# Performance work log

Measured on AMD Instinct MI355X. Metric: run time of the kernel, lower is better.

Reference implementation:

```python
import jax, jax.numpy as jnp
import numpy as np

B, S, D, H, K = 16, 4096, 256, 512, 3
EPS = 1e-5


def setup_inputs() -> dict:
    key = jax.random.key(0)
    ks = jax.random.split(key, 16)
    glorot = lambda k, shape: jax.random.uniform(
        k, shape, jnp.float32, -1.0, 1.0) * np.sqrt(6.0 / (shape[0] + shape[-1]))
    return {
        "inputs": jax.random.normal(ks[0], (B, S, D), jnp.float32),
        "mask": jax.random.randint(ks[1], (B, S), 0, 2, jnp.int32),
        "in_w": glorot(ks[2], (H, D)),
        "in_b": jnp.zeros((H,), jnp.float32),
        "gate_w": glorot(ks[3], (H, D)),
        "gate_b": jnp.zeros((H,), jnp.float32),
        "dw_w": glorot(ks[4], (H, 1, K)),
        "dw_b": jnp.zeros((H,), jnp.float32),
        "pw_w": glorot(ks[5], (H, H, 1)),
        "pw_b": jnp.zeros((H,), jnp.float32),
        "ln_g": jnp.ones((H,), jnp.float32),
        "ln_b": jnp.zeros((H,), jnp.float32),
        "A_log": jax.random.normal(ks[6], (H,), jnp.float32) * -0.1,
        "Bp": jax.random.normal(ks[7], (H,), jnp.float32) * 0.1,
        "Cp": jax.random.normal(ks[8], (H,), jnp.float32) * 0.1,
    }


def _forward(inputs, mask, in_w, in_b, gate_w, gate_b, dw_w, dw_b,
             pw_w, pw_b, ln_g, ln_b, A_log, Bp, Cp):
    # projections: torch Linear is x @ W.T + b
    x_lin = jnp.einsum('bsd,hd->bsh', inputs, in_w) + in_b
    g_lin = jnp.einsum('bsd,hd->bsh', inputs, gate_w) + gate_b
    h = jnp.tanh(x_lin)
    m_f = mask.astype(h.dtype)                      # [B,S]
    h = h * m_f[:, :, None]
    # depthwise conv over time: [B,H,S] with groups=H, 'same' padding
    pad = (K - 1) // 2
    h_t = jnp.transpose(h, (0, 2, 1))               # [B,H,S]
    h_conv = jax.lax.conv_general_dilated(
        h_t, dw_w, window_strides=(1,), padding=[(pad, pad)],
        dimension_numbers=('NCH', 'OIH', 'NCH'), feature_group_count=H)
    h_conv = h_conv + dw_b[None, :, None]
    h_conv = jnp.transpose(h_conv, (0, 2, 1))       # [B,S,H]
    # pointwise 1x1 conv
    h_conv = jnp.einsum('bsh,oh->bso', h_conv, pw_w[:, :, 0]) + pw_b
    u = jax.nn.silu(h_conv + h)
    g = jax.nn.sigmoid(g_lin)
    a_exp = jnp.exp(-jax.nn.softplus(A_log))        # [H]

    def step(carry, xs):
        state, last = carry
        ut, gt, mt = xs                             # [B,H],[B,H],[B]
        new_state = gt * (a_exp * state) + (1.0 - gt) * (Bp * ut)
        keep = (mt > 0.5)[:, None]
        state = jnp.where(keep, new_state, state)
        y = state * Cp
        last = jnp.where(keep, y, last)
        return (state, last), last

    init = (jnp.zeros((B, H), u.dtype), jnp.zeros((B, H), u.dtype))
    xs = (jnp.transpose(u, (1, 0, 2)), jnp.transpose(g, (1, 0, 2)),
          jnp.transpose(m_f, (1, 0)))
    _, y_seq = jax.lax.scan(step, init, xs)         # [S,B,H]
    y_seq = jnp.transpose(y_seq, (1, 0, 2))         # [B,S,H]
    # LayerNorm over last dim
    mu = jnp.mean(y_seq, axis=-1, keepdims=True)
    var = jnp.var(y_seq, axis=-1, keepdims=True)
    return (y_seq - mu) * jax.lax.rsqrt(var + EPS) * ln_g + ln_b


def reference(inputs, mask, in_w, in_b, gate_w, gate_b, dw_w, dw_b,
              pw_w, pw_b, ln_g, ln_b, A_log, Bp, Cp):
    return _forward(inputs, mask, in_w, in_b, gate_w, gate_b, dw_w, dw_b,
                    pw_w, pw_b, ln_g, ln_b, A_log, Bp, Cp)
```

## Files before the change

### kernel.cpp

```cpp
#include <hip/hip_runtime.h>
#include <hip/hip_bf16.h>
#include <math.h>

#define B_  16
#define S_  4096
#define D_  256
#define H_  512
#define BS_ 65536
#define BSH_ 33554432L
#define BSD_ 16777216L
#define CCH 128
#define LCH 32
#define TPAD 136

typedef __bf16 bf16;
typedef __bf16 bf16x8 __attribute__((ext_vector_type(8)));
typedef float  f32x4  __attribute__((ext_vector_type(4)));

#define AS1 __attribute__((address_space(1)))
#define AS3 __attribute__((address_space(3)))

__device__ __forceinline__ void gload_lds16(const void* g, void* l) {
  __builtin_amdgcn_global_load_lds((const AS1 void*)g, (AS3 void*)l, 16, 0, 0);
}

#if __has_builtin(__builtin_amdgcn_exp2f)
#define EXP2F __builtin_amdgcn_exp2f
#else
#define EXP2F exp2f
#endif
#if __has_builtin(__builtin_amdgcn_rcpf)
#define RCPF __builtin_amdgcn_rcpf
#else
#define RCPF(x) (1.f/(x))
#endif
#define L2E 1.4426950408889634f

__device__ __forceinline__ float fsigmoid(float x) {
  return RCPF(1.f + EXP2F(-L2E * x));
}
__device__ __forceinline__ float ftanh(float x) {
  return 2.f * RCPF(1.f + EXP2F(-2.f * L2E * x)) - 1.f;
}
__device__ __forceinline__ float fsilu(float x) {
  return x * RCPF(1.f + EXP2F(-L2E * x));
}

__global__ void k_cast_x(const float* __restrict__ x, bf16* __restrict__ xb, int n8) {
  int i = blockIdx.x * blockDim.x + threadIdx.x;
  if (i >= n8) return;
  const float4* p = (const float4*)x + (long)i * 2;
  float4 a = p[0], b = p[1];
  bf16x8 o;
  o[0]=(bf16)a.x; o[1]=(bf16)a.y; o[2]=(bf16)a.z; o[3]=(bf16)a.w;
  o[4]=(bf16)b.x; o[5]=(bf16)b.y; o[6]=(bf16)b.z; o[7]=(bf16)b.w;
  ((bf16x8*)xb)[i] = o;
}

__global__ void k_cast_w(const float* __restrict__ in_w, const float* __restrict__ gate_w,
                         const float* __restrict__ pw_w,
                         bf16* __restrict__ w1, bf16* __restrict__ pw) {
  int i = blockIdx.x * blockDim.x + threadIdx.x;
  const int HD = H_ * D_;
  if (i < HD)            w1[i] = (bf16)in_w[i];
  else if (i < 2 * HD)   w1[i] = (bf16)gate_w[i - HD];
  else {
    int j = i - 2 * HD;
    if (j < H_ * H_)     pw[j] = (bf16)pw_w[j];
  }
}

template<int KDIM, int EPI>
__global__ __launch_bounds__(512, 5)
void k_gemm(const bf16* __restrict__ A, const bf16* __restrict__ Bw,
            const int* __restrict__ mask,
            const float* __restrict__ bias0, const float* __restrict__ bias1,
            const bf16* __restrict__ hbuf, const bf16* __restrict__ gbuf,
            const float* __restrict__ A_log, const float* __restrict__ Bp,
            float* __restrict__ Ac, float* __restrict__ Bc,
            bf16* __restrict__ out0, bf16* __restrict__ out1, int Ntiles)
{
  extern __shared__ char smem_raw[];
  bf16* tile = (bf16*)smem_raw;

  const int t = threadIdx.x;
  const int w = t >> 6, lane = t & 63;
  const int nwg = gridDim.x;
  const int wg = (blockIdx.x & 7) * (nwg >> 3) + (blockIdx.x >> 3);
  const int bn0 = (wg % Ntiles) * 128;
  const int bm0 = (wg / Ntiles) * 128;
  const int wm = w >> 2, wn = w & 3;
  const int fr = lane & 15, kq = lane >> 4;
  constexpr int NT = KDIM / 32;

  const bf16* Ag = A  + (long)(bm0 + (t >> 2)) * KDIM + (t & 3) * 8;
  const bf16* Bg = Bw + (long)(bn0 + (t >> 2)) * KDIM + (t & 3) * 8;

  f32x4 acc[4][2];
#pragma unroll
  for (int i = 0; i < 4; ++i)
#pragma unroll
    for (int j = 0; j < 2; ++j) acc[i][j] = (f32x4){0.f, 0.f, 0.f, 0.f};

#define STAGE(tt)                                                           \
  { char* _b = smem_raw + ((tt) & 1) * 16384;                               \
    gload_lds16(Ag + (tt) * 32, (bf16*)_b + t * 8);                         \
    gload_lds16(Bg + (tt) * 32, (bf16*)(_b + 8192) + t * 8); }

  STAGE(0); STAGE(1);

#pragma unroll
  for (int kt = 0; kt < NT; ++kt) {
    if (kt + 1 < NT) asm volatile("s_waitcnt vmcnt(2)" ::: "memory");
    else             asm volatile("s_waitcnt vmcnt(0)" ::: "memory");
    __builtin_amdgcn_s_barrier();

    const bf16* As = (const bf16*)(smem_raw + (kt & 1) * 16384);
    const bf16* Bs = As + 4096;
    bf16x8 af[4], bfr[2];
#pragma unroll
    for (int mi = 0; mi < 4; ++mi)
      af[mi] = *(const bf16x8*)&As[(wm * 64 + mi * 16 + fr) * 32 + kq * 8];
#pragma unroll
    for (int ni = 0; ni < 2; ++ni)
      bfr[ni] = *(const bf16x8*)&Bs[(wn * 32 + ni * 16 + fr) * 32 + kq * 8];

    asm volatile("s_waitcnt lgkmcnt(0)" ::: "memory");
    __builtin_amdgcn_s_barrier();

    if (kt + 2 < NT) STAGE(kt + 2);

#pragma unroll
    for (int mi = 0; mi < 4; ++mi)
#pragma unroll
      for (int ni = 0; ni < 2; ++ni)
        acc[mi][ni] = __builtin_amdgcn_mfma_f32_16x16x32_bf16(af[mi], bfr[ni], acc[mi][ni], 0, 0, 0);
  }
#undef STAGE

  __syncthreads();

  const bool hside = (EPI != 1) || (bn0 < H_);
#pragma unroll
  for (int mi = 0; mi < 4; ++mi) {
#pragma unroll
    for (int rr = 0; rr < 4; ++rr) {
      const int row = wm * 64 + mi * 16 + kq * 4 + rr;
      const int gm = bm0 + row;
      float mf = 1.f;
      if (EPI == 1) mf = (mask[gm] != 0) ? 1.f : 0.f;
#pragma unroll
      for (int ni = 0; ni < 2; ++ni) {
        const int col = wn * 32 + ni * 16 + fr;
        float c = acc[mi][ni][rr];
        float val;
        if (EPI == 1) {
          const int gn = bn0 + col;
          val = hside ? ftanh(c + bias0[gn]) * mf
                      : fsigmoid(c + bias1[gn - H_]);
        } else {
          val = c + bias0[bn0 + col];
        }
        tile[row * TPAD + col] = (bf16)val;
      }
    }
  }
  __syncthreads();

  const int pr = t >> 4;
  const int pc = (t & 15) * 8;
#pragma unroll
  for (int rr = 0; rr < 4; ++rr) {
    const int row = pr + rr * 32;
    const long gm = bm0 + row;
    bf16x8 v = *(const bf16x8*)&tile[row * TPAD + pc];
    if (EPI == 1) {
      if (hside) *(bf16x8*)&out0[gm * H_ + bn0 + pc] = v;
      else       *(bf16x8*)&out1[gm * H_ + (bn0 - H_) + pc] = v;
    } else {
      bf16x8 hb = *(const bf16x8*)&hbuf[gm * H_ + bn0 + pc];
      bf16x8 o;
#pragma unroll
      for (int k = 0; k < 8; ++k) {
        float s = (float)v[k] + (float)hb[k];
        o[k] = (bf16)fsilu(s);
      }
      *(bf16x8*)&out0[gm * H_ + bn0 + pc] = o;
      *(bf16x8*)&tile[row * TPAD + pc] = o;
    }
  }

  if constexpr (EPI == 2) {
    __syncthreads();
    const int c_idx = t >> 7;
    const int col   = t & 127;
    const int gcol  = bn0 + col;
    const int bIdx  = bm0 >> 12;
    const int s0    = bm0 & (S_ - 1);
    const int chunk = (s0 >> 5) + c_idx;
    const int* mrow = mask + bIdx * S_ + s0 + c_idx * 32;
    const float aexp = RCPF(1.f + EXP2F(L2E * A_log[gcol]));
    const float bp = Bp[gcol];
    const bf16* grow = gbuf + (long)(bm0 + c_idx * 32) * H_ + gcol;
    float At = 1.f, Bt = 0.f;
#pragma unroll 4
    for (int sl = 0; sl < LCH; ++sl) {
      float uv = (float)tile[(c_idx * 32 + sl) * TPAD + col];
      float gv = (float)grow[(long)sl * H_];
      bool mm = mrow[sl] != 0;
      float a_s = mm ? gv * aexp : 1.f;
      float b_s = mm ? (1.f - gv) * (bp * uv) : 0.f;
      At = a_s * At;
      Bt = fmaf(a_s, Bt, b_s);
    }
    long o = ((long)chunk * B_ + bIdx) * H_ + gcol;
    Ac[o] = At; Bc[o] = Bt;
  }
}

__global__ void k_dwconv(const bf16* __restrict__ h, const float* __restrict__ dww,
                         const float* __restrict__ dwb, bf16* __restrict__ hc)
{
  long idx = (long)blockIdx.x * blockDim.x + threadIdx.x;
  long m = idx >> 6;
  int h8 = ((int)idx & 63) << 3;
  int s = (int)(m & (S_ - 1));
  bf16x8 c0, c1, c2;
#pragma unroll
  for (int j = 0; j < 8; ++j) { c0[j] = (bf16)0.f; c2[j] = (bf16)0.f; }
  if (s > 0)        c0 = *(const bf16x8*)(h + (m - 1) * H_ + h8);
  c1 = *(const bf16x8*)(h + m * H_ + h8);
  if (s < S_ - 1)   c2 = *(const bf16x8*)(h + (m + 1) * H_ + h8);
  bf16x8 o;
#pragma unroll
  for (int j = 0; j < 8; ++j) {
    int hh = h8 + j;
    float v = (float)c0[j] * dww[hh * 3 + 0] + (float)c1[j] * dww[hh * 3 + 1]
            + (float)c2[j] * dww[hh * 3 + 2] + dwb[hh];
    o[j] = (bf16)v;
  }
  *(bf16x8*)(hc + m * H_ + h8) = o;
}


__global__ __launch_bounds__(256)
void k_scan2(const float* __restrict__ Ac, const float* __restrict__ Bc,
             float* __restrict__ Sin)
{
  int tid = blockIdx.x * 256 + threadIdx.x;
  int b = tid >> 9, h = tid & (H_ - 1);
  const long stride = (long)B_ * H_;
  long o = (long)b * H_ + h;
  float st = 0.f;
  float a = Ac[o], bb = Bc[o];
  for (int c = 0; c < CCH; ++c) {
    float an = 0.f, bn = 0.f;
    if (c + 1 < CCH) { an = Ac[o + stride]; bn = Bc[o + stride]; }
    Sin[o] = st;
    st = fmaf(a, st, bb);
    a = an; bb = bn; o += stride;
  }
}

__global__ __launch_bounds__(256)
void k_scan3(const bf16* __restrict__ u, const bf16* __restrict__ g,
             const int* __restrict__ mask, const float* __restrict__ A_log,
             const float* __restrict__ Bp, const float* __restrict__ Cp,
             const float* __restrict__ Sin,
             const float* __restrict__ ln_g, const float* __restrict__ ln_b,
             float* __restrict__ out)
{
  const int wv = threadIdx.x >> 6, lane = threadIdx.x & 63;
  const int c = blockIdx.x * 4 + wv;
  const int b = blockIdx.y;
  const int h0 = lane * 8;

  float aexp[8], bp[8], cp[8], lg[8], lb[8], st[8];
#pragma unroll
  for (int j = 0; j < 8; ++j) {
    aexp[j] = RCPF(1.f + EXP2F(L2E * A_log[h0 + j]));
    bp[j] = Bp[h0 + j]; cp[j] = Cp[h0 + j];
    lg[j] = ln_g[h0 + j]; lb[j] = ln_b[h0 + j];
    st[j] = Sin[((long)c * B_ + b) * H_ + h0 + j];
  }

  const long base = ((long)b * S_ + (long)c * LCH) * H_ + h0;
  const int* mrow = mask + b * S_ + c * LCH;

  bf16x8 uv = *(const bf16x8*)(u + base);
  bf16x8 gv = *(const bf16x8*)(g + base);
  int mm = mrow[0];

  for (int sl = 0; sl < LCH; ++sl) {
    bf16x8 un, gn; int mn = 0;
    if (sl + 1 < LCH) {
      un = *(const bf16x8*)(u + base + (long)(sl + 1) * H_);
      gn = *(const bf16x8*)(g + base + (long)(sl + 1) * H_);
      mn = mrow[sl + 1];
    }
    const bool m = mm != 0;
    float y[8], sum = 0.f, sq = 0.f;
#pragma unroll
    for (int j = 0; j < 8; ++j) {
      float uu = (float)uv[j], gg = (float)gv[j];
      float a_s = m ? gg * aexp[j] : 1.f;
      float b_s = m ? (1.f - gg) * (bp[j] * uu) : 0.f;
      st[j] = fmaf(a_s, st[j], b_s);
      y[j] = st[j] * cp[j];
      sum += y[j];
      sq = fmaf(y[j], y[j], sq);
    }
#pragma unroll
    for (int off = 32; off; off >>= 1) {
      sum += __shfl_xor(sum, off);
      sq  += __shfl_xor(sq, off);
    }
    const float mu = sum * (1.f / H_);
    const float var = sq * (1.f / H_) - mu * mu;
    const float rs = rsqrtf(var + 1e-5f);
    const long ob = base + (long)sl * H_;
    f32x4 o0, o1;
#pragma unroll
    for (int j = 0; j < 4; ++j) o0[j] = (y[j] - mu) * rs * lg[j] + lb[j];
#pragma unroll
    for (int j = 0; j < 4; ++j) o1[j] = (y[4 + j] - mu) * rs * lg[4 + j] + lb[4 + j];
    *(f32x4*)(out + ob) = o0;
    *(f32x4*)(out + ob + 4) = o1;
    uv = un; gv = gn; mm = mn;
  }
}

extern "C" void kernel_launch(void* const* d_in, const int* in_sizes, int n_in,
                              void* d_out, int out_size, void* d_ws, size_t ws_size,
                              hipStream_t stream)
{
  const float* x      = (const float*)d_in[0];
  const int*   mask   = (const int*)d_in[1];
  const float* in_w   = (const float*)d_in[2];
  const float* in_b   = (const float*)d_in[3];
  const float* gate_w = (const float*)d_in[4];
  const float* gate_b = (const float*)d_in[5];
  const float* dw_w   = (const float*)d_in[6];
  const float* dw_b   = (const float*)d_in[7];
  const float* pw_w   = (const float*)d_in[8];
  const float* pw_b   = (const float*)d_in[9];
  const float* ln_g   = (const float*)d_in[10];
  const float* ln_b   = (const float*)d_in[11];
  const float* A_log  = (const float*)d_in[12];
  const float* Bp     = (const float*)d_in[13];
  const float* Cp     = (const float*)d_in[14];

  char* ws = (char*)d_ws;
  bf16*  xb  = (bf16*)(ws + 0L);
  bf16*  h   = (bf16*)(ws + 33554432L);
  bf16*  hc  = (bf16*)(ws + 100663296L);
  bf16*  u   = (bf16*)(ws + 167772160L);
  bf16*  g   = (bf16*)(ws + 234881024L);
  bf16*  w1  = (bf16*)(ws + 301989888L);
  bf16*  pw  = (bf16*)(ws + 302514176L);
  float* Ac  = (float*)(ws + 303038464L);
  float* Bc  = (float*)(ws + 307232768L);
  float* Sin = (float*)(ws + 311427072L);
  float* out = (float*)d_out;

  const int gemm_lds = 128 * TPAD * 2;

  k_cast_x<<<8192, 256, 0, stream>>>(x, xb, (int)(BSD_ / 8));
  k_cast_w<<<2048, 256, 0, stream>>>(in_w, gate_w, pw_w, w1, pw);
  k_gemm<256, 1><<<512 * 8, 512, gemm_lds, stream>>>(
      xb, w1, mask, in_b, gate_b, nullptr, nullptr, nullptr, nullptr,
      nullptr, nullptr, h, g, 8);
  k_dwconv<<<16384, 256, 0, stream>>>(h, dw_w, dw_b, hc);
  k_gemm<512, 2><<<512 * 4, 512, gemm_lds, stream>>>(
      hc, pw, mask, pw_b, nullptr, h, g, A_log, Bp,
      Ac, Bc, u, nullptr, 4);
  k_scan2<<<32, 256, 0, stream>>>(Ac, Bc, Sin);
  k_scan3<<<dim3(CCH / 4, B_), 256, 0, stream>>>(
      u, g, mask, A_log, Bp, Cp, Sin, ln_g, ln_b, out);
}
```

Before: 326.4 us.

## Double GEMM K-step to 64 with k-sliced LDS layout

The GEMM main loop now processes 64 K elements per stage instead of 32, halving the number of barrier/wait iterations. The LDS tile layout becomes k-slice-major (8-element columns, 128 rows contiguous) to avoid bank conflicts on fragment reads. LDS per block goes to 64KB and launch bounds drop to 4 waves per SIMD, which lowers occupancy in exchange for fewer synchronisations per FLOP.

```diff
diff --git a/kernel.cpp b/kernel.cpp
--- a/kernel.cpp
+++ b/kernel.cpp
@@ -71,7 +71,7 @@
 }
 
 template<int KDIM, int EPI>
-__global__ __launch_bounds__(512, 5)
+__global__ __launch_bounds__(512, 4)
 void k_gemm(const bf16* __restrict__ A, const bf16* __restrict__ Bw,
             const int* __restrict__ mask,
             const float* __restrict__ bias0, const float* __restrict__ bias1,
@@ -91,10 +91,13 @@
   const int bm0 = (wg / Ntiles) * 128;
   const int wm = w >> 2, wn = w & 3;
   const int fr = lane & 15, kq = lane >> 4;
-  constexpr int NT = KDIM / 32;
-
-  const bf16* Ag = A  + (long)(bm0 + (t >> 2)) * KDIM + (t & 3) * 8;
-  const bf16* Bg = Bw + (long)(bn0 + (t >> 2)) * KDIM + (t & 3) * 8;
+  constexpr int NT = KDIM / 64;
+
+  const int sr = t & 127, sk = t >> 7;
+  const bf16* Ag = A  + (long)(bm0 + sr) * KDIM + sk * 8;
+  const bf16* Bg = Bw + (long)(bn0 + sr) * KDIM + sk * 8;
+  bf16* const L0 = (bf16*)smem_raw + sk * 1024 + sr * 8;
+  bf16* const L1 = L0 + 4096;
 
   f32x4 acc[4][2];
 #pragma unroll
@@ -103,27 +106,33 @@
     for (int j = 0; j < 2; ++j) acc[i][j] = (f32x4){0.f, 0.f, 0.f, 0.f};
 
 #define STAGE(tt)                                                           \
-  { char* _b = smem_raw + ((tt) & 1) * 16384;                               \
-    gload_lds16(Ag + (tt) * 32, (bf16*)_b + t * 8);                         \
-    gload_lds16(Bg + (tt) * 32, (bf16*)(_b + 8192) + t * 8); }
+  { const int _p = ((tt) & 1) * 16384;                                      \
+    gload_lds16(Ag + (tt) * 64,      L0 + _p);                              \
+    gload_lds16(Ag + (tt) * 64 + 32, L1 + _p);                              \
+    gload_lds16(Bg + (tt) * 64,      L0 + 8192 + _p);                       \
+    gload_lds16(Bg + (tt) * 64 + 32, L1 + 8192 + _p); }
 
   STAGE(0); STAGE(1);
 
 #pragma unroll
   for (int kt = 0; kt < NT; ++kt) {
-    if (kt + 1 < NT) asm volatile("s_waitcnt vmcnt(2)" ::: "memory");
+    if (kt + 1 < NT) asm volatile("s_waitcnt vmcnt(4)" ::: "memory");
     else             asm volatile("s_waitcnt vmcnt(0)" ::: "memory");
     __builtin_amdgcn_s_barrier();
 
-    const bf16* As = (const bf16*)(smem_raw + (kt & 1) * 16384);
-    const bf16* Bs = As + 4096;
-    bf16x8 af[4], bfr[2];
-#pragma unroll
-    for (int mi = 0; mi < 4; ++mi)
-      af[mi] = *(const bf16x8*)&As[(wm * 64 + mi * 16 + fr) * 32 + kq * 8];
-#pragma unroll
-    for (int ni = 0; ni < 2; ++ni)
-      bfr[ni] = *(const bf16x8*)&Bs[(wn * 32 + ni * 16 + fr) * 32 + kq * 8];
+    const bf16* As = (const bf16*)smem_raw + (kt & 1) * 16384;
+    const bf16* Bs = As + 8192;
+    bf16x8 af[4][2], bfr[2][2];
+#pragma unroll
+    for (int kk = 0; kk < 2; ++kk) {
+      const int ks = (kk * 4 + kq) * 1024;
+#pragma unroll
+      for (int mi = 0; mi < 4; ++mi)
+        af[mi][kk] = *(const bf16x8*)&As[ks + (wm * 64 + mi * 16 + fr) * 8];
+#pragma unroll
+      for (int ni = 0; ni < 2; ++ni)
+        bfr[ni][kk] = *(const bf16x8*)&Bs[ks + (wn * 32 + ni * 16 + fr) * 8];
+    }
 
     asm volatile("s_waitcnt lgkmcnt(0)" ::: "memory");
     __builtin_amdgcn_s_barrier();
@@ -131,10 +140,12 @@
     if (kt + 2 < NT) STAGE(kt + 2);
 
 #pragma unroll
-    for (int mi = 0; mi < 4; ++mi)
-#pragma unroll
-      for (int ni = 0; ni < 2; ++ni)
-        acc[mi][ni] = __builtin_amdgcn_mfma_f32_16x16x32_bf16(af[mi], bfr[ni], acc[mi][ni], 0, 0, 0);
+    for (int kk = 0; kk < 2; ++kk)
+#pragma unroll
+      for (int mi = 0; mi < 4; ++mi)
+#pragma unroll
+        for (int ni = 0; ni < 2; ++ni)
+          acc[mi][ni] = __builtin_amdgcn_mfma_f32_16x16x32_bf16(af[mi][kk], bfr[ni][kk], acc[mi][ni], 0, 0, 0);
   }
 #undef STAGE
 
@@ -363,7 +374,7 @@
   float* Sin = (float*)(ws + 311427072L);
   float* out = (float*)d_out;
 
-  const int gemm_lds = 128 * TPAD * 2;
+  const int gemm_lds = 65536;
 
   k_cast_x<<<8192, 256, 0, stream>>>(x, xb, (int)(BSD_ / 8));
   k_cast_w<<<2048, 256, 0, stream>>>(in_w, gate_w, pw_w, w1, pw);
```

Measured after the change: 406.0 us. 1.24x slower.

## Shrink GEMM N-tile to 64 with XOR-swizzled LDS and higher occupancy

Applied to the files above, without the earlier changes.

Both GEMM kernels now use 128x64 output tiles instead of 128x128, doubling the grid and halving the per-block LDS footprint so launch bounds can request 8 blocks per CU. The LDS staging layout is XOR-swizzled on the K-quad index to reduce bank conflicts on fragment reads. The fused scan epilogue is restricted to half the threads to match the narrower tile. The smaller N tile lowers reuse of the A tile and doubles A-matrix global reads, which is traded for occupancy and load balance.

```diff
diff --git a/kernel.cpp b/kernel.cpp
--- a/kernel.cpp
+++ b/kernel.cpp
@@ -11,7 +11,7 @@
 #define BSD_ 16777216L
 #define CCH 128
 #define LCH 32
-#define TPAD 136
+#define TP  72
 
 typedef __bf16 bf16;
 typedef __bf16 bf16x8 __attribute__((ext_vector_type(8)));
@@ -71,7 +71,7 @@
 }
 
 template<int KDIM, int EPI>
-__global__ __launch_bounds__(512, 5)
+__global__ __launch_bounds__(512, 8)
 void k_gemm(const bf16* __restrict__ A, const bf16* __restrict__ Bw,
             const int* __restrict__ mask,
             const float* __restrict__ bias0, const float* __restrict__ bias1,
@@ -87,43 +87,46 @@
   const int w = t >> 6, lane = t & 63;
   const int nwg = gridDim.x;
   const int wg = (blockIdx.x & 7) * (nwg >> 3) + (blockIdx.x >> 3);
-  const int bn0 = (wg % Ntiles) * 128;
+  const int bn0 = (wg % Ntiles) * 64;
   const int bm0 = (wg / Ntiles) * 128;
   const int wm = w >> 2, wn = w & 3;
   const int fr = lane & 15, kq = lane >> 4;
+  const int kqs = (kq ^ (fr & 3)) << 3;
   constexpr int NT = KDIM / 32;
 
-  const bf16* Ag = A  + (long)(bm0 + (t >> 2)) * KDIM + (t & 3) * 8;
-  const bf16* Bg = Bw + (long)(bn0 + (t >> 2)) * KDIM + (t & 3) * 8;
-
-  f32x4 acc[4][2];
-#pragma unroll
-  for (int i = 0; i < 4; ++i)
-#pragma unroll
-    for (int j = 0; j < 2; ++j) acc[i][j] = (f32x4){0.f, 0.f, 0.f, 0.f};
-
-#define STAGE(tt)                                                           \
-  { char* _b = smem_raw + ((tt) & 1) * 16384;                               \
-    gload_lds16(Ag + (tt) * 32, (bf16*)_b + t * 8);                         \
-    gload_lds16(Bg + (tt) * 32, (bf16*)(_b + 8192) + t * 8); }
+  const int sr = t >> 2;
+  const int sq = (t & 3) ^ (sr & 3);
+  const bf16* Ag = A  + (long)(bm0 + sr) * KDIM + sq * 8;
+  const bf16* Bg = Bw + (long)(bn0 + sr) * KDIM + sq * 8;
+
+  f32x4 acc[4];
+#pragma unroll
+  for (int i = 0; i < 4; ++i) acc[i] = (f32x4){0.f, 0.f, 0.f, 0.f};
+
+#define STAGE(tt)                                                            \
+  { bf16* _b = (bf16*)smem_raw + ((tt) & 1) * 6144;                          \
+    gload_lds16(Ag + (tt) * 32, _b + t * 8);                                 \
+    if (t < 256) gload_lds16(Bg + (tt) * 32, _b + 4096 + t * 8); }
 
   STAGE(0); STAGE(1);
 
 #pragma unroll
   for (int kt = 0; kt < NT; ++kt) {
-    if (kt + 1 < NT) asm volatile("s_waitcnt vmcnt(2)" ::: "memory");
-    else             asm volatile("s_waitcnt vmcnt(0)" ::: "memory");
+    if (kt + 1 < NT) {
+      if (w < 4) asm volatile("s_waitcnt vmcnt(2)" ::: "memory");
+      else       asm volatile("s_waitcnt vmcnt(1)" ::: "memory");
+    } else {
+      asm volatile("s_waitcnt vmcnt(0)" ::: "memory");
+    }
     __builtin_amdgcn_s_barrier();
 
-    const bf16* As = (const bf16*)(smem_raw + (kt & 1) * 16384);
+    const bf16* As = (const bf16*)smem_raw + (kt & 1) * 6144;
     const bf16* Bs = As + 4096;
-    bf16x8 af[4], bfr[2];
+    bf16x8 af[4], bfr;
 #pragma unroll
     for (int mi = 0; mi < 4; ++mi)
-      af[mi] = *(const bf16x8*)&As[(wm * 64 + mi * 16 + fr) * 32 + kq * 8];
-#pragma unroll
-    for (int ni = 0; ni < 2; ++ni)
-      bfr[ni] = *(const bf16x8*)&Bs[(wn * 32 + ni * 16 + fr) * 32 + kq * 8];
+      af[mi] = *(const bf16x8*)&As[(wm * 64 + mi * 16 + fr) * 32 + kqs];
+    bfr = *(const bf16x8*)&Bs[(wn * 16 + fr) * 32 + kqs];
 
     asm volatile("s_waitcnt lgkmcnt(0)" ::: "memory");
     __builtin_amdgcn_s_barrier();
@@ -132,15 +135,14 @@
 
 #pragma unroll
     for (int mi = 0; mi < 4; ++mi)
-#pragma unroll
-      for (int ni = 0; ni < 2; ++ni)
-        acc[mi][ni] = __builtin_amdgcn_mfma_f32_16x16x32_bf16(af[mi], bfr[ni], acc[mi][ni], 0, 0, 0);
+      acc[mi] = __builtin_amdgcn_mfma_f32_16x16x32_bf16(af[mi], bfr, acc[mi], 0, 0, 0);
   }
 #undef STAGE
 
   __syncthreads();
 
   const bool hside = (EPI != 1) || (bn0 < H_);
+  const int col = wn * 16 + fr;
 #pragma unroll
   for (int mi = 0; mi < 4; ++mi) {
 #pragma unroll
@@ -149,31 +151,27 @@
       const int gm = bm0 + row;
       float mf = 1.f;
       if (EPI == 1) mf = (mask[gm] != 0) ? 1.f : 0.f;
-#pragma unroll
-      for (int ni = 0; ni < 2; ++ni) {
-        const int col = wn * 32 + ni * 16 + fr;
-        float c = acc[mi][ni][rr];
-        float val;
-        if (EPI == 1) {
-          const int gn = bn0 + col;
-          val = hside ? ftanh(c + bias0[gn]) * mf
-                      : fsigmoid(c + bias1[gn - H_]);
-        } else {
-          val = c + bias0[bn0 + col];
-        }
-        tile[row * TPAD + col] = (bf16)val;
+      float c = acc[mi][rr];
+      float val;
+      if (EPI == 1) {
+        const int gn = bn0 + col;
+        val = hside ? ftanh(c + bias0[gn]) * mf
+                    : fsigmoid(c + bias1[gn - H_]);
+      } else {
+        val = c + bias0[bn0 + col];
       }
+      tile[row * TP + col] = (bf16)val;
     }
   }
   __syncthreads();
 
-  const int pr = t >> 4;
-  const int pc = (t & 15) * 8;
-#pragma unroll
-  for (int rr = 0; rr < 4; ++rr) {
-    const int row = pr + rr * 32;
+  const int pr = t >> 3;
+  const int pc = (t & 7) * 8;
+#pragma unroll
+  for (int rr = 0; rr < 2; ++rr) {
+    const int row = pr + rr * 64;
     const long gm = bm0 + row;
-    bf16x8 v = *(const bf16x8*)&tile[row * TPAD + pc];
+    bf16x8 v = *(const bf16x8*)&tile[row * TP + pc];
     if (EPI == 1) {
       if (hside) *(bf16x8*)&out0[gm * H_ + bn0 + pc] = v;
       else       *(bf16x8*)&out1[gm * H_ + (bn0 - H_) + pc] = v;
@@ -186,35 +184,37 @@
         o[k] = (bf16)fsilu(s);
       }
       *(bf16x8*)&out0[gm * H_ + bn0 + pc] = o;
-      *(bf16x8*)&tile[row * TPAD + pc] = o;
+      *(bf16x8*)&tile[row * TP + pc] = o;
     }
   }
 
   if constexpr (EPI == 2) {
     __syncthreads();
-    const int c_idx = t >> 7;
-    const int col   = t & 127;
-    const int gcol  = bn0 + col;
-    const int bIdx  = bm0 >> 12;
-    const int s0    = bm0 & (S_ - 1);
-    const int chunk = (s0 >> 5) + c_idx;
-    const int* mrow = mask + bIdx * S_ + s0 + c_idx * 32;
-    const float aexp = RCPF(1.f + EXP2F(L2E * A_log[gcol]));
-    const float bp = Bp[gcol];
-    const bf16* grow = gbuf + (long)(bm0 + c_idx * 32) * H_ + gcol;
-    float At = 1.f, Bt = 0.f;
+    if (t < 256) {
+      const int c_idx = t >> 6;
+      const int scol  = t & 63;
+      const int gcol  = bn0 + scol;
+      const int bIdx  = bm0 >> 12;
+      const int s0    = bm0 & (S_ - 1);
+      const int chunk = (s0 >> 5) + c_idx;
+      const int* mrow = mask + bIdx * S_ + s0 + c_idx * 32;
+      const float aexp = RCPF(1.f + EXP2F(L2E * A_log[gcol]));
+      const float bp = Bp[gcol];
+      const bf16* grow = gbuf + (long)(bm0 + c_idx * 32) * H_ + gcol;
+      float At = 1.f, Bt = 0.f;
 #pragma unroll 4
-    for (int sl = 0; sl < LCH; ++sl) {
-      float uv = (float)tile[(c_idx * 32 + sl) * TPAD + col];
-      float gv = (float)grow[(long)sl * H_];
-      bool mm = mrow[sl] != 0;
-      float a_s = mm ? gv * aexp : 1.f;
-      float b_s = mm ? (1.f - gv) * (bp * uv) : 0.f;
-      At = a_s * At;
-      Bt = fmaf(a_s, Bt, b_s);
-    }
-    long o = ((long)chunk * B_ + bIdx) * H_ + gcol;
-    Ac[o] = At; Bc[o] = Bt;
+      for (int sl = 0; sl < LCH; ++sl) {
+        float uv = (float)tile[(c_idx * 32 + sl) * TP + scol];
+        float gv = (float)grow[(long)sl * H_];
+        bool mm = mrow[sl] != 0;
+        float a_s = mm ? gv * aexp : 1.f;
+        float b_s = mm ? (1.f - gv) * (bp * uv) : 0.f;
+        At = a_s * At;
+        Bt = fmaf(a_s, Bt, b_s);
+      }
+      long o = ((long)chunk * B_ + bIdx) * H_ + gcol;
+      Ac[o] = At; Bc[o] = Bt;
+    }
   }
 }
 
@@ -241,7 +241,6 @@
   }
   *(bf16x8*)(hc + m * H_ + h8) = o;
 }
-
 
 __global__ __launch_bounds__(256)
 void k_scan2(const float* __restrict__ Ac, const float* __restrict__ Bc,
@@ -363,17 +362,17 @@
   float* Sin = (float*)(ws + 311427072L);
   float* out = (float*)d_out;
 
-  const int gemm_lds = 128 * TPAD * 2;
+  const int gemm_lds = 24576;
 
   k_cast_x<<<8192, 256, 0, stream>>>(x, xb, (int)(BSD_ / 8));
   k_cast_w<<<2048, 256, 0, stream>>>(in_w, gate_w, pw_w, w1, pw);
-  k_gemm<256, 1><<<512 * 8, 512, gemm_lds, stream>>>(
+  k_gemm<256, 1><<<512 * 16, 512, gemm_lds, stream>>>(
       xb, w1, mask, in_b, gate_b, nullptr, nullptr, nullptr, nullptr,
-      nullptr, nullptr, h, g, 8);
+      nullptr, nullptr, h, g, 16);
   k_dwconv<<<16384, 256, 0, stream>>>(h, dw_w, dw_b, hc);
-  k_gemm<512, 2><<<512 * 4, 512, gemm_lds, stream>>>(
+  k_gemm<512, 2><<<512 * 8, 512, gemm_lds, stream>>>(
       hc, pw, mask, pw_b, nullptr, h, g, A_log, Bp,
-      Ac, Bc, u, nullptr, 4);
+      Ac, Bc, u, nullptr, 8);
   k_scan2<<<32, 256, 0, stream>>>(Ac, Bc, Sin);
   k_scan3<<<dim3(CCH / 4, B_), 256, 0, stream>>>(
       u, g, mask, A_log, Bp, Cp, Sin, ln_g, ln_b, out);
```

After: 333.2 us. 2.1% more time.

## Add weight-stationary GEMM kernel for the input/gate projection

Applied to the files above, without the earlier changes.

Adds a new GEMM kernel that keeps a 64-column slice of the combined in/gate weight in LDS for the whole workgroup. Each wave streams 16-row A fragments straight from global memory into registers and issues bf16 MFMAs against that resident weight. The epilogue writes tanh/mask or sigmoid results through a small per-wave LDS staging buffer so global stores are coalesced. This replaces the earlier tiled k_gemm for the first projection, removing repeated weight tile loads. In exchange, A is read with no LDS reuse and the grid is much smaller.

```diff
diff --git a/kernel.cpp b/kernel.cpp
--- a/kernel.cpp
+++ b/kernel.cpp
@@ -7,7 +7,6 @@
 #define D_  256
 #define H_  512
 #define BS_ 65536
-#define BSH_ 33554432L
 #define BSD_ 16777216L
 #define CCH 128
 #define LCH 32
@@ -68,6 +67,112 @@
     int j = i - 2 * HD;
     if (j < H_ * H_)     pw[j] = (bf16)pw_w[j];
   }
+}
+
+template<int KDIM, int EPI, int NBLK, int NCH, int NCOL>
+__global__ __launch_bounds__(512, 4)
+void k_wgemm(const bf16* __restrict__ A, const bf16* __restrict__ Bw,
+             const int* __restrict__ mask,
+             const float* __restrict__ bias0, const float* __restrict__ bias1,
+             bf16* __restrict__ out0, bf16* __restrict__ out1)
+{
+  constexpr int NF  = NCOL / 16;
+  constexpr int SCS = NCOL + 8;
+  constexpr int K8  = KDIM / 8;
+  constexpr int NT  = KDIM / 32;
+
+  extern __shared__ char smem[];
+  bf16* Wl = (bf16*)smem;
+  const int t = threadIdx.x;
+  const int w8 = t >> 6, lane = t & 63;
+  bf16* sc = (bf16*)(smem + (long)NCOL * KDIM * 2 + w8 * (8 * SCS * 2));
+
+  const int nwg = gridDim.x;
+  const int wg = (blockIdx.x & 7) * (nwg >> 3) + (blockIdx.x >> 3);
+  const int n0 = (wg % NBLK) * NCOL;
+  const int ms = wg / NBLK;
+  const long wbase = (long)ms * (16L * 8 * NCH) + (long)w8 * (16 * NCH);
+
+  for (int i = t; i < NCOL * K8; i += 512) {
+    const int k8 = i & (K8 - 1), c = i / K8;
+    *(bf16x8*)(Wl + k8 * (NCOL * 8) + c * 8) =
+        *(const bf16x8*)(Bw + (long)(n0 + c) * KDIM + k8 * 8);
+  }
+  __syncthreads();
+
+  const int fr = lane & 15, kq = lane >> 4;
+  const bool hside = (EPI != 1) || (n0 < H_);
+
+  float b0[NF], b1g[NF];
+#pragma unroll
+  for (int nf = 0; nf < NF; ++nf) {
+    const int c = n0 + nf * 16 + fr;
+    b0[nf]  = hside ? bias0[c] : 0.f;
+    b1g[nf] = (!hside) ? bias1[c - H_] : 0.f;
+  }
+
+  bf16x8 af[NT];
+#define LOADA(m0_)                                                          \
+  { const bf16* _p = A + ((m0_) + fr) * (long)KDIM + kq * 8;                \
+    _Pragma("unroll")                                                       \
+    for (int kt = 0; kt < NT; ++kt) af[kt] = *(const bf16x8*)(_p + kt * 32); }
+
+  LOADA(wbase);
+  for (int ch = 0; ch < NCH; ++ch) {
+    const long m0 = wbase + ch * 16;
+    f32x4 acc[NF];
+#pragma unroll
+    for (int nf = 0; nf < NF; ++nf) acc[nf] = (f32x4){0.f, 0.f, 0.f, 0.f};
+#pragma unroll
+    for (int kt = 0; kt < NT; ++kt) {
+#pragma unroll
+      for (int nf = 0; nf < NF; ++nf) {
+        const bf16x8 bfr =
+            *(const bf16x8*)&Wl[(kt * 4 + kq) * (NCOL * 8) + (nf * 16 + fr) * 8];
+        acc[nf] = __builtin_amdgcn_mfma_f32_16x16x32_bf16(af[kt], bfr, acc[nf], 0, 0, 0);
+      }
+    }
+    if (ch + 1 < NCH) LOADA(m0 + 16);
+
+#pragma unroll
+    for (int p = 0; p < 2; ++p) {
+      const long gr0 = m0 + p * 8;
+      if ((kq >> 1) == p) {
+        const int lr = (kq & 1) * 4;
+#pragma unroll
+        for (int rr = 0; rr < 4; ++rr) {
+          const int row = lr + rr;
+          float mf = 1.f;
+          if (EPI == 1) mf = (mask[gr0 + row] != 0) ? 1.f : 0.f;
+#pragma unroll
+          for (int nf = 0; nf < NF; ++nf) {
+            const float c = acc[nf][rr];
+            float val;
+            if (EPI == 1) val = hside ? ftanh(c + b0[nf]) * mf
+                                      : fsigmoid(c + b1g[nf]);
+            else          val = c + b0[nf];
+            sc[row * SCS + nf * 16 + fr] = (bf16)val;
+          }
+        }
+      }
+      asm volatile("s_waitcnt lgkmcnt(0)" ::: "memory");
+      __builtin_amdgcn_sched_barrier(0);
+      {
+        const int ngr = NCOL / 8;
+        const bool act = (lane < 8 * ngr);
+        const int prow = lane / ngr, pcol = (lane % ngr) * 8;
+        if (act) {
+          const long gm = gr0 + prow;
+          bf16x8 v = *(const bf16x8*)&sc[prow * SCS + pcol];
+          if (hside) *(bf16x8*)&out0[gm * H_ + n0 + pcol] = v;
+          else       *(bf16x8*)&out1[gm * H_ + (n0 - H_) + pcol] = v;
+        }
+      }
+      asm volatile("s_waitcnt lgkmcnt(0)" ::: "memory");
+      __builtin_amdgcn_sched_barrier(0);
+    }
+  }
+#undef LOADA
 }
 
 template<int KDIM, int EPI>
@@ -242,7 +347,6 @@
   *(bf16x8*)(hc + m * H_ + h8) = o;
 }
 
-
 __global__ __launch_bounds__(256)
 void k_scan2(const float* __restrict__ Ac, const float* __restrict__ Bc,
              float* __restrict__ Sin)
@@ -363,17 +467,18 @@
   float* Sin = (float*)(ws + 311427072L);
   float* out = (float*)d_out;
 
-  const int gemm_lds = 128 * TPAD * 2;
-
   k_cast_x<<<8192, 256, 0, stream>>>(x, xb, (int)(BSD_ / 8));
   k_cast_w<<<2048, 256, 0, stream>>>(in_w, gate_w, pw_w, w1, pw);
-  k_gemm<256, 1><<<512 * 8, 512, gemm_lds, stream>>>(
-      xb, w1, mask, in_b, gate_b, nullptr, nullptr, nullptr, nullptr,
-      nullptr, nullptr, h, g, 8);
+
+  k_wgemm<256, 1, 16, 16, 64><<<512, 512, 41984, stream>>>(
+      xb, w1, mask, in_b, gate_b, h, g);
+
   k_dwconv<<<16384, 256, 0, stream>>>(h, dw_w, dw_b, hc);
-  k_gemm<512, 2><<<512 * 4, 512, gemm_lds, stream>>>(
+
+  k_gemm<512, 2><<<512 * 4, 512, 34816, stream>>>(
       hc, pw, mask, pw_b, nullptr, h, g, A_log, Bp,
       Ac, Bc, u, nullptr, 4);
+
   k_scan2<<<32, 256, 0, stream>>>(Ac, Bc, Sin);
   k_scan3<<<dim3(CCH / 4, B_), 256, 0, stream>>>(
       u, g, mask, A_log, Bp, Cp, Sin, ln_g, ln_b, out);
```

Result: slower. 355.2 us (+8.8%).
